# Kernel optimization log

Measured on AMD Instinct MI355X. Metric: run time of the kernel, lower is better.

Reference implementation:

```python
import jax, jax.numpy as jnp
import numpy as np

N, E, D, H = 100000, 640000, 128, 256


def _mlp(x, w1, b1, w2, b2, w3, b3):
    x = jax.nn.relu(x @ w1.T + b1)
    x = jax.nn.relu(x @ w2.T + b2)
    return x @ w3.T + b3


def _gru(x, h, wih, whh, bih, bhh):
    gi = x @ wih.T + bih
    gh = h @ whh.T + bhh
    ir, iz, inn = jnp.split(gi, 3, axis=-1)
    hr, hz, hn = jnp.split(gh, 3, axis=-1)
    r = jax.nn.sigmoid(ir + hr)
    z = jax.nn.sigmoid(iz + hz)
    n = jnp.tanh(inn + r * hn)
    return (1.0 - z) * n + z * h


def setup_inputs() -> dict:
    key = jax.random.key(0)
    ks = jax.random.split(key, 24)
    s = lambda *shape: 0.05
    inp = {
        "node_states": jax.random.normal(ks[0], (N, D), jnp.float32),
        "edge_features": jax.random.normal(ks[1], (E, D), jnp.float32),
        "from_idx": jax.random.randint(ks[2], (E,), 0, N, jnp.int64 if jax.config.jax_enable_x64 else jnp.int32),
        "to_idx": jax.random.randint(ks[3], (E,), 0, N, jnp.int64 if jax.config.jax_enable_x64 else jnp.int32),
        "graph_idx": jax.random.randint(ks[4], (N,), 0, 16, jnp.int32),
        # message_net MLP params
        "w1": jax.random.normal(ks[5], (H, 3 * D), jnp.float32) * 0.05,
        "b1": jnp.zeros((H,), jnp.float32),
        "w2": jax.random.normal(ks[6], (H, H), jnp.float32) * 0.05,
        "b2": jnp.zeros((H,), jnp.float32),
        "w3": jax.random.normal(ks[7], (D, H), jnp.float32) * 0.05,
        "b3": jnp.zeros((D,), jnp.float32),
    }
    # three GRU cells
    for i in range(3):
        inp[f"g{i}_wih"] = jax.random.normal(ks[8 + 4 * i], (3 * D, D), jnp.float32) * 0.05
        inp[f"g{i}_whh"] = jax.random.normal(ks[9 + 4 * i], (3 * D, D), jnp.float32) * 0.05
        inp[f"g{i}_bih"] = jnp.zeros((3 * D,), jnp.float32)
        inp[f"g{i}_bhh"] = jnp.zeros((3 * D,), jnp.float32)
    return inp


def _prop_once(node_states, f_idx, t_idx, edge_features, w1, b1, w2, b2, w3, b3):
    from_states = node_states[f_idx]  # [E, D]
    to_states = node_states[t_idx]    # [E, D]
    edge_inputs = jnp.concatenate([from_states, to_states, edge_features], axis=1)  # [E, 3D]
    edge_states = _mlp(edge_inputs, w1, b1, w2, b2, w3, b3)  # [E, D]
    return jax.ops.segment_sum(edge_states, t_idx, num_segments=node_states.shape[0])


def reference(node_states, edge_features, from_idx, to_idx, graph_idx,
              w1, b1, w2, b2, w3, b3,
              g0_wih, g0_whh, g0_bih, g0_bhh,
              g1_wih, g1_whh, g1_bih, g1_bhh,
              g2_wih, g2_whh, g2_bih, g2_bhh):
    # both directions use self.message_net in the original forward
    agg = _prop_once(node_states, from_idx, to_idx, edge_features, w1, b1, w2, b2, w3, b3)
    agg = agg + _prop_once(node_states, to_idx, from_idx, edge_features, w1, b1, w2, b2, w3, b3)
    s1 = _gru(node_states, agg, g0_wih, g0_whh, g0_bih, g0_bhh)
    s2 = _gru(agg, s1, g1_wih, g1_whh, g1_bih, g1_bhh)
    s3 = _gru(s1, s2, g2_wih, g2_whh, g2_bih, g2_bhh)
    return s3
```

## Files before the change

### kernel.cpp

```cpp
#include <hip/hip_runtime.h>

#define NN 100000
#define NE 640000
#define D 128
#define HH 256
#define TD 384

typedef __bf16 bf16x8 __attribute__((ext_vector_type(8)));
typedef float f32x4 __attribute__((ext_vector_type(4)));

__device__ __forceinline__ unsigned short f2bf(float f) {
    unsigned u = __builtin_bit_cast(unsigned, f);
    u += 0x7FFFu + ((u >> 16) & 1u);
    return (unsigned short)(u >> 16);
}

__global__ void cvt8_kernel(const float* __restrict__ src,
                            unsigned short* __restrict__ dst, int n8) {
    int i = blockIdx.x * 256 + threadIdx.x;
    if (i >= n8) return;
    const float4* s = (const float4*)(src + (size_t)i * 8);
    float4 a = s[0], b = s[1];
    uint4 pk;
    pk.x = f2bf(a.x) | ((unsigned)f2bf(a.y) << 16);
    pk.y = f2bf(a.z) | ((unsigned)f2bf(a.w) << 16);
    pk.z = f2bf(b.x) | ((unsigned)f2bf(b.y) << 16);
    pk.w = f2bf(b.z) | ((unsigned)f2bf(b.w) << 16);
    *(uint4*)(dst + (size_t)i * 8) = pk;
}

template<bool PRE>
__global__ __launch_bounds__(256, 4) void edge_mlp_v4(
    const float* __restrict__ ns, const float* __restrict__ ef,
    const unsigned short* __restrict__ nsb,
    const int* __restrict__ fidx, const int* __restrict__ tidx,
    const unsigned short* __restrict__ w1b, const float* __restrict__ b1,
    const unsigned short* __restrict__ w2b, const float* __restrict__ b2,
    const unsigned short* __restrict__ w3b, const float* __restrict__ b3,
    float* __restrict__ agg)
{
    __shared__ __align__(16) unsigned short smem[64 * 256];
    __shared__ int sF[32], sT[32];

    const int tid = threadIdx.x;
    const int e0 = blockIdx.x * 32;
    if (tid < 32) { sF[tid] = fidx[e0 + tid]; sT[tid] = tidx[e0 + tid]; }
    __syncthreads();

    const int w  = tid >> 6;
    const int l  = tid & 63;
    const int lr = l & 15;
    const int lk = l >> 4;

    if (PRE) {
        #pragma unroll
        for (int i = 0; i < 4; i++) {
            int gid = tid + i * 256;
            int c = gid >> 4;
            int s = gid & 15;
            int edge = c & 31;
            const unsigned short* src = nsb + (size_t)((c < 32) ? sF[edge] : sT[edge]) * 128;
            uint4 v = *(const uint4*)(src + s * 8);
            *(uint4*)(smem + c * 128 + ((s * 8) ^ ((edge & 7) << 3))) = v;
        }
    } else {
        const int kk0 = (tid & 7) * 16;
        for (int c = tid >> 3; c < 64; c += 32) {
            const int edge = c & 31;
            const float* src = (c < 32) ? ns + (size_t)sF[edge] * D
                                        : ns + (size_t)sT[edge] * D;
            unsigned short* cb = smem + c * 128;
            #pragma unroll
            for (int g = 0; g < 2; g++) {
                float4 a = *(const float4*)(src + kk0 + g * 8);
                float4 b = *(const float4*)(src + kk0 + g * 8 + 4);
                uint4 pk;
                pk.x = f2bf(a.x) | ((unsigned)f2bf(a.y) << 16);
                pk.y = f2bf(a.z) | ((unsigned)f2bf(a.w) << 16);
                pk.z = f2bf(b.x) | ((unsigned)f2bf(b.y) << 16);
                pk.w = f2bf(b.z) | ((unsigned)f2bf(b.w) << 16);
                int sw = (kk0 + g * 8) ^ ((edge & 7) << 3);
                *(uint4*)(cb + sw) = pk;
            }
        }
    }
    {
        const int row = tid >> 3;
        const int kk0 = (tid & 7) * 16;
        const float* src = ef + (size_t)(e0 + row) * D;
        unsigned short* cb = smem + (64 + row) * 128;
        #pragma unroll
        for (int g = 0; g < 2; g++) {
            float4 a = *(const float4*)(src + kk0 + g * 8);
            float4 b = *(const float4*)(src + kk0 + g * 8 + 4);
            uint4 pk;
            pk.x = f2bf(a.x) | ((unsigned)f2bf(a.y) << 16);
            pk.y = f2bf(a.z) | ((unsigned)f2bf(a.w) << 16);
            pk.z = f2bf(b.x) | ((unsigned)f2bf(b.y) << 16);
            pk.w = f2bf(b.z) | ((unsigned)f2bf(b.w) << 16);
            int sw = (kk0 + g * 8) ^ ((row & 7) << 3);
            *(uint4*)(cb + sw) = pk;
        }
    }
    __syncthreads();

    f32x4 acc1[4][4];
    #pragma unroll
    for (int mt = 0; mt < 4; mt++)
        #pragma unroll
        for (int ct = 0; ct < 4; ct++) acc1[mt][ct] = (f32x4){0.f, 0.f, 0.f, 0.f};

    for (int kc = 0; kc < 12; kc++) {
        const int gk = kc * 32;
        const int c128 = gk >> 7;
        const int kk = (gk & 127) + lk * 8;
        bf16x8 af[4];
        #pragma unroll
        for (int mt = 0; mt < 4; mt++) {
            int edge = ((mt & 1) << 4) + lr;
            int dir = mt >> 1;
            int part = dir ? (c128 == 0 ? 1 : (c128 == 1 ? 0 : 2)) : c128;
            int idx = (part * 32 + edge) * 128 + (kk ^ ((edge & 7) << 3));
            af[mt] = *(const bf16x8*)(smem + idx);
        }
        #pragma unroll
        for (int ct = 0; ct < 4; ct++) {
            int col = (w * 4 + ct) * 16 + lr;
            bf16x8 bfr = *(const bf16x8*)(w1b + col * TD + gk + lk * 8);
            #pragma unroll
            for (int mt = 0; mt < 4; mt++)
                acc1[mt][ct] = __builtin_amdgcn_mfma_f32_16x16x32_bf16(af[mt], bfr, acc1[mt][ct], 0, 0, 0);
        }
    }
    __syncthreads();

    #pragma unroll
    for (int ct = 0; ct < 4; ct++) {
        int col = (w * 4 + ct) * 16 + lr;
        float bias = b1[col];
        #pragma unroll
        for (int mt = 0; mt < 4; mt++)
            #pragma unroll
            for (int j = 0; j < 4; j++) {
                int row = mt * 16 + lk * 4 + j;
                float v = acc1[mt][ct][j] + bias;
                v = v > 0.f ? v : 0.f;
                smem[row * 256 + (col ^ ((row & 7) << 3))] = f2bf(v);
            }
    }
    __syncthreads();

    f32x4 acc2[4][4];
    #pragma unroll
    for (int mt = 0; mt < 4; mt++)
        #pragma unroll
        for (int ct = 0; ct < 4; ct++) acc2[mt][ct] = (f32x4){0.f, 0.f, 0.f, 0.f};

    for (int kc = 0; kc < 8; kc++) {
        const int k = kc * 32 + lk * 8;
        bf16x8 af[4];
        #pragma unroll
        for (int mt = 0; mt < 4; mt++) {
            int row = mt * 16 + lr;
            af[mt] = *(const bf16x8*)(smem + row * 256 + (k ^ ((row & 7) << 3)));
        }
        #pragma unroll
        for (int ct = 0; ct < 4; ct++) {
            int col = (w * 4 + ct) * 16 + lr;
            bf16x8 bfr = *(const bf16x8*)(w2b + col * 256 + k);
            #pragma unroll
            for (int mt = 0; mt < 4; mt++)
                acc2[mt][ct] = __builtin_amdgcn_mfma_f32_16x16x32_bf16(af[mt], bfr, acc2[mt][ct], 0, 0, 0);
        }
    }
    __syncthreads();
    #pragma unroll
    for (int ct = 0; ct < 4; ct++) {
        int col = (w * 4 + ct) * 16 + lr;
        float bias = b2[col];
        #pragma unroll
        for (int mt = 0; mt < 4; mt++)
            #pragma unroll
            for (int j = 0; j < 4; j++) {
                int row = mt * 16 + lk * 4 + j;
                float v = acc2[mt][ct][j] + bias;
                v = v > 0.f ? v : 0.f;
                smem[row * 256 + (col ^ ((row & 7) << 3))] = f2bf(v);
            }
    }
    __syncthreads();

    f32x4 acc3[4][2];
    #pragma unroll
    for (int mt = 0; mt < 4; mt++) { acc3[mt][0] = (f32x4){0.f,0.f,0.f,0.f}; acc3[mt][1] = (f32x4){0.f,0.f,0.f,0.f}; }

    for (int kc = 0; kc < 8; kc++) {
        const int k = kc * 32 + lk * 8;
        bf16x8 af[4];
        #pragma unroll
        for (int mt = 0; mt < 4; mt++) {
            int row = mt * 16 + lr;
            af[mt] = *(const bf16x8*)(smem + row * 256 + (k ^ ((row & 7) << 3)));
        }
        #pragma unroll
        for (int ct = 0; ct < 2; ct++) {
            int col = (w * 2 + ct) * 16 + lr;
            bf16x8 bfr = *(const bf16x8*)(w3b + col * 256 + k);
            #pragma unroll
            for (int mt = 0; mt < 4; mt++)
                acc3[mt][ct] = __builtin_amdgcn_mfma_f32_16x16x32_bf16(af[mt], bfr, acc3[mt][ct], 0, 0, 0);
        }
    }

    #pragma unroll
    for (int ct = 0; ct < 2; ct++) {
        int d = (w * 2 + ct) * 16 + lr;
        float bias = b3[d];
        #pragma unroll
        for (int mt = 0; mt < 4; mt++)
            #pragma unroll
            for (int j = 0; j < 4; j++) {
                int edge = ((mt & 1) << 4) + lk * 4 + j;
                int node = (mt >> 1) ? sF[edge] : sT[edge];
                atomicAdd(agg + (size_t)node * D + d, acc3[mt][ct][j] + bias);
            }
    }
}

__global__ __launch_bounds__(256, 2) void gru_kernel(
    const float* __restrict__ x, const float* __restrict__ h,
    const unsigned short* __restrict__ wihb, const unsigned short* __restrict__ whhb,
    const float* __restrict__ bih, const float* __restrict__ bhh,
    float* __restrict__ out)
{
    __shared__ __align__(16) unsigned short xb[32 * 128];
    __shared__ __align__(16) unsigned short hb[32 * 128];
    const int tid = threadIdx.x;
    const size_t r0 = (size_t)blockIdx.x * 32;

    {
        const int row = tid >> 3;
        const int kk0 = (tid & 7) * 16;
        const float* sx = x + (r0 + row) * D + kk0;
        const float* sh = h + (r0 + row) * D + kk0;
        #pragma unroll
        for (int g = 0; g < 2; g++) {
            float4 a = *(const float4*)(sx + g * 8);
            float4 b = *(const float4*)(sx + g * 8 + 4);
            uint4 pk;
            pk.x = f2bf(a.x) | ((unsigned)f2bf(a.y) << 16);
            pk.y = f2bf(a.z) | ((unsigned)f2bf(a.w) << 16);
            pk.z = f2bf(b.x) | ((unsigned)f2bf(b.y) << 16);
            pk.w = f2bf(b.z) | ((unsigned)f2bf(b.w) << 16);
            int sw = (kk0 + g * 8) ^ ((row & 7) << 3);
            *(uint4*)(xb + row * 128 + sw) = pk;
            a = *(const float4*)(sh + g * 8);
            b = *(const float4*)(sh + g * 8 + 4);
            pk.x = f2bf(a.x) | ((unsigned)f2bf(a.y) << 16);
            pk.y = f2bf(a.z) | ((unsigned)f2bf(a.w) << 16);
            pk.z = f2bf(b.x) | ((unsigned)f2bf(b.y) << 16);
            pk.w = f2bf(b.z) | ((unsigned)f2bf(b.w) << 16);
            *(uint4*)(hb + row * 128 + sw) = pk;
        }
    }
    __syncthreads();

    const int w = tid >> 6, l = tid & 63, lr = l & 15, lk = l >> 4;

    f32x4 agi[2][3][2], agh[2][3][2];
    #pragma unroll
    for (int mt = 0; mt < 2; mt++)
        #pragma unroll
        for (int g = 0; g < 3; g++)
            #pragma unroll
            for (int t = 0; t < 2; t++) {
                agi[mt][g][t] = (f32x4){0.f,0.f,0.f,0.f};
                agh[mt][g][t] = (f32x4){0.f,0.f,0.f,0.f};
            }

    for (int kc = 0; kc < 4; kc++) {
        const int k = kc * 32 + lk * 8;
        bf16x8 ax[2], ah[2];
        #pragma unroll
        for (int mt = 0; mt < 2; mt++) {
            int row = mt * 16 + lr;
            int idx = row * 128 + (k ^ ((row & 7) << 3));
            ax[mt] = *(const bf16x8*)(xb + idx);
            ah[mt] = *(const bf16x8*)(hb + idx);
        }
        #pragma unroll
        for (int g = 0; g < 3; g++)
            #pragma unroll
            for (int t = 0; t < 2; t++) {
                int col = g * 128 + (w * 2 + t) * 16 + lr;
                bf16x8 bi = *(const bf16x8*)(wihb + col * 128 + k);
                bf16x8 bh = *(const bf16x8*)(whhb + col * 128 + k);
                #pragma unroll
                for (int mt = 0; mt < 2; mt++) {
                    agi[mt][g][t] = __builtin_amdgcn_mfma_f32_16x16x32_bf16(ax[mt], bi, agi[mt][g][t], 0, 0, 0);
                    agh[mt][g][t] = __builtin_amdgcn_mfma_f32_16x16x32_bf16(ah[mt], bh, agh[mt][g][t], 0, 0, 0);
                }
            }
    }

    #pragma unroll
    for (int t = 0; t < 2; t++) {
        const int d = (w * 2 + t) * 16 + lr;
        const float bir = bih[d], biz = bih[D + d], bin_ = bih[2 * D + d];
        const float bhr = bhh[d], bhz = bhh[D + d], bhn = bhh[2 * D + d];
        #pragma unroll
        for (int mt = 0; mt < 2; mt++)
            #pragma unroll
            for (int j = 0; j < 4; j++) {
                size_t row = r0 + mt * 16 + lk * 4 + j;
                float hv = h[row * D + d];
                float rr = agi[mt][0][t][j] + bir + agh[mt][0][t][j] + bhr;
                float zz = agi[mt][1][t][j] + biz + agh[mt][1][t][j] + bhz;
                float ni = agi[mt][2][t][j] + bin_;
                float nh = agh[mt][2][t][j] + bhn;
                float r_ = 1.f / (1.f + __expf(-rr));
                float z_ = 1.f / (1.f + __expf(-zz));
                float n_ = tanhf(ni + r_ * nh);
                out[row * D + d] = (1.f - z_) * n_ + z_ * hv;
            }
    }
}

extern "C" void kernel_launch(void* const* d_in, const int* in_sizes, int n_in,
                              void* d_out, int out_size, void* d_ws, size_t ws_size,
                              hipStream_t stream)
{
    const float* ns = (const float*)d_in[0];
    const float* ef = (const float*)d_in[1];
    const int*   fidx = (const int*)d_in[2];
    const int*   tidx = (const int*)d_in[3];
    const float* w1 = (const float*)d_in[5];
    const float* b1 = (const float*)d_in[6];
    const float* w2 = (const float*)d_in[7];
    const float* b2 = (const float*)d_in[8];
    const float* w3 = (const float*)d_in[9];
    const float* b3 = (const float*)d_in[10];
    const float* gwih_f[3] = {(const float*)d_in[11], (const float*)d_in[15], (const float*)d_in[19]};
    const float* gwhh_f[3] = {(const float*)d_in[12], (const float*)d_in[16], (const float*)d_in[20]};
    const float* gbih[3]   = {(const float*)d_in[13], (const float*)d_in[17], (const float*)d_in[21]};
    const float* gbhh[3]   = {(const float*)d_in[14], (const float*)d_in[18], (const float*)d_in[22]};

    char* ws = (char*)d_ws;
    float* agg = (float*)ws;
    float* s1  = (float*)(ws + (size_t)NN * D * 4);
    unsigned short* w1b = (unsigned short*)(ws + (size_t)2 * NN * D * 4);
    unsigned short* w2b = w1b + 256 * 384;
    unsigned short* w3b = w2b + 256 * 256;
    unsigned short* gwih[3];
    unsigned short* gwhh[3];
    unsigned short* p = w3b + 128 * 256;
    for (int i = 0; i < 3; i++) { gwih[i] = p; p += 384 * 128; gwhh[i] = p; p += 384 * 128; }
    unsigned short* nsb = p;
    size_t needed = (size_t)((char*)(nsb + (size_t)NN * D) - ws);
    const bool pre = (ws_size >= needed);

    auto cvt = [&](const float* s, unsigned short* dst, size_t n) {
        int n8 = (int)(n / 8);
        cvt8_kernel<<<(n8 + 255) / 256, 256, 0, stream>>>(s, dst, n8);
    };
    cvt(w1, w1b, 256 * 384);
    cvt(w2, w2b, 256 * 256);
    cvt(w3, w3b, 128 * 256);
    for (int i = 0; i < 3; i++) { cvt(gwih_f[i], gwih[i], 384 * 128); cvt(gwhh_f[i], gwhh[i], 384 * 128); }
    if (pre) cvt(ns, nsb, (size_t)NN * D);

    hipMemsetAsync(agg, 0, (size_t)NN * D * 4, stream);

    if (pre)
        edge_mlp_v4<true><<<NE / 32, 256, 0, stream>>>(ns, ef, nsb, fidx, tidx, w1b, b1, w2b, b2, w3b, b3, agg);
    else
        edge_mlp_v4<false><<<NE / 32, 256, 0, stream>>>(ns, ef, nsb, fidx, tidx, w1b, b1, w2b, b2, w3b, b3, agg);

    float* s2 = (float*)d_out;
    gru_kernel<<<NN / 32, 256, 0, stream>>>(ns,  agg, gwih[0], gwhh[0], gbih[0], gbhh[0], s1);
    gru_kernel<<<NN / 32, 256, 0, stream>>>(agg, s1,  gwih[1], gwhh[1], gbih[1], gbhh[1], s2);
    gru_kernel<<<NN / 32, 256, 0, stream>>>(s1,  s2,  gwih[2], gwhh[2], gbih[2], gbhh[2], (float*)d_out);
}
```

Baseline: 2.032 ms.

## Replace atomic scatter with CSR-sorted gather aggregation of bf16 edge messages

Builds a CSR index of edge-direction messages per destination node using count, scan and fill kernels. The edge MLP now writes per-edge bf16 messages instead of doing float atomicAdds. A separate kernel then sums each node's messages without atomics. This removes heavy atomic contention on the aggregation buffer. In exchange it adds extra kernels, large intermediate message traffic, a bigger workspace requirement, and bf16 rounding of the messages.

```diff
diff --git a/kernel.cpp b/kernel.cpp
--- a/kernel.cpp
+++ b/kernel.cpp
@@ -5,6 +5,7 @@
 #define D 128
 #define HH 256
 #define TD 384
+#define NCHUNK 391
 
 typedef __bf16 bf16x8 __attribute__((ext_vector_type(8)));
 typedef float f32x4 __attribute__((ext_vector_type(4)));
@@ -29,15 +30,79 @@
     *(uint4*)(dst + (size_t)i * 8) = pk;
 }
 
+__global__ void k_count(const int* __restrict__ fidx, const int* __restrict__ tidx,
+                        int* __restrict__ cnt) {
+    int e = blockIdx.x * 256 + threadIdx.x;
+    if (e >= NE) return;
+    atomicAdd(&cnt[tidx[e]], 1);
+    atomicAdd(&cnt[fidx[e]], 1);
+}
+
+__global__ void k_scan1(const int* __restrict__ cnt, int* __restrict__ bsum) {
+    __shared__ int red[256];
+    int t = threadIdx.x, i = blockIdx.x * 256 + t;
+    int v = (i < NN) ? cnt[i] : 0;
+    red[t] = v; __syncthreads();
+    for (int off = 128; off > 0; off >>= 1) {
+        if (t < off) red[t] += red[t + off];
+        __syncthreads();
+    }
+    if (t == 0) bsum[blockIdx.x] = red[0];
+}
+
+__global__ void k_scan2(int* __restrict__ bsum, int* __restrict__ starts) {
+    __shared__ int sc[512];
+    int t = threadIdx.x;
+    int v = (t < NCHUNK) ? bsum[t] : 0;
+    sc[t] = v; __syncthreads();
+    for (int off = 1; off < 512; off <<= 1) {
+        int x = (t >= off) ? sc[t - off] : 0;
+        __syncthreads();
+        sc[t] += x;
+        __syncthreads();
+    }
+    if (t < NCHUNK) bsum[t] = sc[t] - v;
+    if (t == 0) starts[NN] = 2 * NE;
+}
+
+__global__ void k_scan3(int* __restrict__ cnt, const int* __restrict__ bsum,
+                        int* __restrict__ starts) {
+    __shared__ int sc[256];
+    int t = threadIdx.x, i = blockIdx.x * 256 + t;
+    int v = (i < NN) ? cnt[i] : 0;
+    sc[t] = v; __syncthreads();
+    for (int off = 1; off < 256; off <<= 1) {
+        int x = (t >= off) ? sc[t - off] : 0;
+        __syncthreads();
+        sc[t] += x;
+        __syncthreads();
+    }
+    if (i < NN) {
+        int ex = bsum[blockIdx.x] + sc[t] - v;
+        starts[i] = ex;
+        cnt[i] = ex;
+    }
+}
+
+__global__ void k_fill(const int* __restrict__ fidx, const int* __restrict__ tidx,
+                       int* __restrict__ cursor, unsigned* __restrict__ perm) {
+    int e = blockIdx.x * 256 + threadIdx.x;
+    if (e >= NE) return;
+    int p0 = atomicAdd(&cursor[tidx[e]], 1);
+    perm[p0] = (unsigned)e;
+    int p1 = atomicAdd(&cursor[fidx[e]], 1);
+    perm[p1] = (unsigned)e | 0x80000000u;
+}
+
 template<bool PRE>
-__global__ __launch_bounds__(256, 4) void edge_mlp_v4(
+__global__ __launch_bounds__(256, 4) void edge_mlp_v5(
     const float* __restrict__ ns, const float* __restrict__ ef,
     const unsigned short* __restrict__ nsb,
     const int* __restrict__ fidx, const int* __restrict__ tidx,
     const unsigned short* __restrict__ w1b, const float* __restrict__ b1,
     const unsigned short* __restrict__ w2b, const float* __restrict__ b2,
     const unsigned short* __restrict__ w3b, const float* __restrict__ b3,
-    float* __restrict__ agg)
+    unsigned short* __restrict__ msg, float* __restrict__ agg, bool use_atomic)
 {
     __shared__ __align__(16) unsigned short smem[64 * 256];
     __shared__ int sF[32], sT[32];
@@ -212,19 +277,58 @@
         }
     }
 
-    #pragma unroll
-    for (int ct = 0; ct < 2; ct++) {
-        int d = (w * 2 + ct) * 16 + lr;
-        float bias = b3[d];
-        #pragma unroll
-        for (int mt = 0; mt < 4; mt++)
-            #pragma unroll
-            for (int j = 0; j < 4; j++) {
-                int edge = ((mt & 1) << 4) + lk * 4 + j;
-                int node = (mt >> 1) ? sF[edge] : sT[edge];
-                atomicAdd(agg + (size_t)node * D + d, acc3[mt][ct][j] + bias);
-            }
-    }
+    if (use_atomic) {
+        #pragma unroll
+        for (int ct = 0; ct < 2; ct++) {
+            int d = (w * 2 + ct) * 16 + lr;
+            float bias = b3[d];
+            #pragma unroll
+            for (int mt = 0; mt < 4; mt++)
+                #pragma unroll
+                for (int j = 0; j < 4; j++) {
+                    int edge = ((mt & 1) << 4) + lk * 4 + j;
+                    int node = (mt >> 1) ? sF[edge] : sT[edge];
+                    atomicAdd(agg + (size_t)node * D + d, acc3[mt][ct][j] + bias);
+                }
+        }
+    } else {
+        #pragma unroll
+        for (int ct = 0; ct < 2; ct++) {
+            int d = (w * 2 + ct) * 16 + lr;
+            float bias = b3[d];
+            #pragma unroll
+            for (int mt = 0; mt < 4; mt++) {
+                int dir = mt >> 1;
+                #pragma unroll
+                for (int j = 0; j < 4; j++) {
+                    int edge = ((mt & 1) << 4) + lk * 4 + j;
+                    size_t row = (size_t)dir * NE + (e0 + edge);
+                    msg[row * 128 + d] = f2bf(acc3[mt][ct][j] + bias);
+                }
+            }
+        }
+    }
+}
+
+__global__ __launch_bounds__(256, 4) void k_agg(
+    const unsigned short* __restrict__ msg, const unsigned* __restrict__ perm,
+    const int* __restrict__ starts, float* __restrict__ agg)
+{
+    const int node = blockIdx.x * 4 + (threadIdx.x >> 6);
+    if (node >= NN) return;
+    const int l = threadIdx.x & 63;
+    const int s = starts[node];
+    const int e = starts[node + 1];
+    const int d2 = l * 2;
+    float a0 = 0.f, a1 = 0.f;
+    for (int i = s; i < e; i++) {
+        unsigned enc = perm[i];
+        size_t row = (size_t)(enc & 0x7FFFFFFFu) + (size_t)(enc >> 31) * NE;
+        unsigned v = *(const unsigned*)(msg + row * 128 + d2);
+        a0 += __builtin_bit_cast(float, v << 16);
+        a1 += __builtin_bit_cast(float, v & 0xFFFF0000u);
+    }
+    *(float2*)(agg + (size_t)node * 128 + d2) = make_float2(a0, a1);
 }
 
 __global__ __launch_bounds__(256, 2) void gru_kernel(
@@ -356,8 +460,17 @@
     unsigned short* p = w3b + 128 * 256;
     for (int i = 0; i < 3; i++) { gwih[i] = p; p += 384 * 128; gwhh[i] = p; p += 384 * 128; }
     unsigned short* nsb = p;
-    size_t needed = (size_t)((char*)(nsb + (size_t)NN * D) - ws);
-    const bool pre = (ws_size >= needed);
+    size_t need_pre = (size_t)((char*)(nsb + (size_t)NN * D) - ws);
+
+    unsigned short* msg = nsb + (size_t)NN * D;
+    unsigned* perm = (unsigned*)(msg + (size_t)2 * NE * 128);
+    int* starts = (int*)(perm + (size_t)2 * NE);
+    int* cursor = starts + (NN + 4);
+    int* bsum   = cursor + NN;
+    size_t need_csr = (size_t)((char*)(bsum + 512) - ws);
+
+    const bool pre = (ws_size >= need_pre);
+    const bool csr = (ws_size >= need_csr);
 
     auto cvt = [&](const float* s, unsigned short* dst, size_t n) {
         int n8 = (int)(n / 8);
@@ -369,12 +482,25 @@
     for (int i = 0; i < 3; i++) { cvt(gwih_f[i], gwih[i], 384 * 128); cvt(gwhh_f[i], gwhh[i], 384 * 128); }
     if (pre) cvt(ns, nsb, (size_t)NN * D);
 
-    hipMemsetAsync(agg, 0, (size_t)NN * D * 4, stream);
-
-    if (pre)
-        edge_mlp_v4<true><<<NE / 32, 256, 0, stream>>>(ns, ef, nsb, fidx, tidx, w1b, b1, w2b, b2, w3b, b3, agg);
-    else
-        edge_mlp_v4<false><<<NE / 32, 256, 0, stream>>>(ns, ef, nsb, fidx, tidx, w1b, b1, w2b, b2, w3b, b3, agg);
+    if (csr) {
+        hipMemsetAsync(cursor, 0, NN * 4, stream);
+        k_count<<<(NE + 255) / 256, 256, 0, stream>>>(fidx, tidx, cursor);
+        k_scan1<<<NCHUNK, 256, 0, stream>>>(cursor, bsum);
+        k_scan2<<<1, 512, 0, stream>>>(bsum, starts);
+        k_scan3<<<NCHUNK, 256, 0, stream>>>(cursor, bsum, starts);
+        k_fill<<<(NE + 255) / 256, 256, 0, stream>>>(fidx, tidx, cursor, perm);
+        if (pre)
+            edge_mlp_v5<true><<<NE / 32, 256, 0, stream>>>(ns, ef, nsb, fidx, tidx, w1b, b1, w2b, b2, w3b, b3, msg, agg, false);
+        else
+            edge_mlp_v5<false><<<NE / 32, 256, 0, stream>>>(ns, ef, nsb, fidx, tidx, w1b, b1, w2b, b2, w3b, b3, msg, agg, false);
+        k_agg<<<NN / 4 + 1, 256, 0, stream>>>(msg, perm, starts, agg);
+    } else {
+        hipMemsetAsync(agg, 0, (size_t)NN * D * 4, stream);
+        if (pre)
+            edge_mlp_v5<true><<<NE / 32, 256, 0, stream>>>(ns, ef, nsb, fidx, tidx, w1b, b1, w2b, b2, w3b, b3, (unsigned short*)agg, agg, true);
+        else
+            edge_mlp_v5<false><<<NE / 32, 256, 0, stream>>>(ns, ef, nsb, fidx, tidx, w1b, b1, w2b, b2, w3b, b3, (unsigned short*)agg, agg, true);
+    }
 
     float* s2 = (float*)d_out;
     gru_kernel<<<NN / 32, 256, 0, stream>>>(ns,  agg, gwih[0], gwhh[0], gbih[0], gbhh[0], s1);
```

New measurement: 2.265 ms. +11.5%, slower.
